# Kernel tuning notes

Hardware: AMD Instinct MI355X
Metric: run time of the kernel (lower is better)

The kernel has to match this reference:

```python
import jax, jax.numpy as jnp
import numpy as np

M, K, N = 32, 8192, 28672

def setup_inputs() -> dict:
    key = jax.random.key(0)
    k1, k2, k3 = jax.random.split(key, 3)
    act = jax.random.normal(k1, (M, K), dtype=jnp.float16)
    # int8 quantized weight, stored as int8 (spec lists int32 for harness compat)
    weight = jax.random.randint(k2, (K, N), -127, 128, dtype=jnp.int8)
    # per-output-channel dequant scale, small positive values typical of fp8/int8 quant
    scale = (jax.random.uniform(k3, (1, N), dtype=jnp.float32) * 0.01 + 1e-4).astype(jnp.float16)
    return {"act": act, "weight": weight, "scale": scale}

def reference(act, weight, scale):
    # grouped_gemm with single group: out[m,n] = (sum_k act[m,k] * w[k,n]) * scale[n]
    # int8 weight is dequantized inline; accumulate in fp32, emit fp16 like the kernel.
    acc = jnp.einsum("mk,kn->mn", act.astype(jnp.float16), weight.astype(jnp.float16),
                     preferred_element_type=jnp.float32)
    out = acc * scale.astype(jnp.float32)
    return out.astype(jnp.float16)
```

## Files before the change

### kernel.cpp

```cpp
#include <hip/hip_runtime.h>
#include <hip/hip_bf16.h>

#define MM 32
#define KK 8192
#define NN 28672
#define NB_COUNT (NN / 64)
#define REGION_BYTES (2048 * 64)

typedef _Float16 half8   __attribute__((ext_vector_type(8)));
typedef __fp16   fp16x2  __attribute__((ext_vector_type(2)));
typedef float    floatx4 __attribute__((ext_vector_type(4)));
typedef int      intx4   __attribute__((ext_vector_type(4)));
typedef unsigned int uintx2 __attribute__((ext_vector_type(2)));

__global__ __launch_bounds__(256) void act_cvt_kernel(
    const float* __restrict__ act, __fp16* __restrict__ act16)
{
    int i = (blockIdx.x * 256 + threadIdx.x) * 4;
    floatx4 v = *(const floatx4*)(act + i);
    fp16x2 lo = __builtin_amdgcn_cvt_pkrtz(v[0], v[1]);
    fp16x2 hi = __builtin_amdgcn_cvt_pkrtz(v[2], v[3]);
    __fp16* o = act16 + i;
    *(fp16x2*)(o)     = lo;
    *(fp16x2*)(o + 2) = hi;
}

__global__ __launch_bounds__(256) void repack_kernel(
    const int* __restrict__ weight, unsigned char* __restrict__ wpack)
{
    const int t    = threadIdx.x;
    const int slot = t & 63;
    const int kg   = t >> 6;
    const int n_base = blockIdx.x * 512 + slot * 8;
    const int k_base = blockIdx.y * 32 + kg * 8;

    const int* rp = weight + (size_t)k_base * NN + n_base;
    intx4 A[8], B[8];
#pragma unroll
    for (int j = 0; j < 8; ++j) {
        A[j] = *(const intx4*)(rp + (size_t)j * NN);
        B[j] = *(const intx4*)(rp + (size_t)j * NN + 4);
    }

    const int kc = k_base >> 11;
    const int s  = (k_base & 2047) >> 5;
    const int nb = n_base >> 6;
    const int wv = (n_base & 63) >> 4;
    const int c0 = n_base & 15;
    unsigned char* op = wpack
        + (((size_t)kc * NB_COUNT + nb) << 17)
        + (s << 11) + (wv << 9) + (kg << 7) + (c0 << 3);

    int d[16];
#pragma unroll
    for (int i = 0; i < 4; ++i) {
        d[2 * i]      = (A[0][i] & 255) | ((A[1][i] & 255) << 8) |
                        ((A[2][i] & 255) << 16) | (A[3][i] << 24);
        d[2 * i + 1]  = (A[4][i] & 255) | ((A[5][i] & 255) << 8) |
                        ((A[6][i] & 255) << 16) | (A[7][i] << 24);
        d[2 * i + 8]  = (B[0][i] & 255) | ((B[1][i] & 255) << 8) |
                        ((B[2][i] & 255) << 16) | (B[3][i] << 24);
        d[2 * i + 9]  = (B[4][i] & 255) | ((B[5][i] & 255) << 8) |
                        ((B[6][i] & 255) << 16) | (B[7][i] << 24);
    }
#pragma unroll
    for (int q = 0; q < 4; ++q) {
        intx4 v = {d[4 * q], d[4 * q + 1], d[4 * q + 2], d[4 * q + 3]};
        *(intx4*)(op + q * 16) = v;
    }
}

template <int KSPLIT>
__global__ __launch_bounds__(256) void gemm_pack_kernel(
    const __fp16*        __restrict__ act16,
    const unsigned char* __restrict__ wpack,
    float*               __restrict__ ws)
{
    const int lane = threadIdx.x & 63;
    const int wave = threadIdx.x >> 6;
    const int col  = lane & 15;
    const int quad = lane >> 4;

    const int nb  = blockIdx.x;
    const int kcb = blockIdx.y;
    const int kc  = kcb * (KK / KSPLIT);
    constexpr int NSTEP = (KK / KSPLIT) / 32;

    const unsigned char* wp = wpack
        + (((size_t)kcb * NB_COUNT + nb) << 17)
        + (wave << 9) + (lane << 3);
    const __fp16* ap0 = act16 + (size_t)col * KK + kc + quad * 8;
    const __fp16* ap1 = ap0 + (size_t)16 * KK;

    floatx4 acc0 = {0.f, 0.f, 0.f, 0.f};
    floatx4 acc1 = {0.f, 0.f, 0.f, 0.f};

    uintx2 wA, wB;
    half8  aA0, aA1, aB0, aB1;

    auto load_step = [&](int s, uintx2& w, half8& a0, half8& a1) {
        w  = *(const uintx2*)(wp + (size_t)s * 2048);
        a0 = *(const half8*)(ap0 + s * 32);
        a1 = *(const half8*)(ap1 + s * 32);
    };

    auto compute_step = [&](uintx2 w, const half8 a0, const half8 a1) {
        const unsigned lo = w[0], hi = w[1];
        int j0 = (int)(lo << 24) >> 24;
        int j1 = (int)(lo << 16) >> 24;
        int j2 = (int)(lo <<  8) >> 24;
        int j3 = (int)lo >> 24;
        int j4 = (int)(hi << 24) >> 24;
        int j5 = (int)(hi << 16) >> 24;
        int j6 = (int)(hi <<  8) >> 24;
        int j7 = (int)hi >> 24;
        fp16x2 p0 = __builtin_amdgcn_cvt_pkrtz((float)j0, (float)j1);
        fp16x2 p1 = __builtin_amdgcn_cvt_pkrtz((float)j2, (float)j3);
        fp16x2 p2 = __builtin_amdgcn_cvt_pkrtz((float)j4, (float)j5);
        fp16x2 p3 = __builtin_amdgcn_cvt_pkrtz((float)j6, (float)j7);
        half8 b;
        b[0] = p0[0]; b[1] = p0[1]; b[2] = p1[0]; b[3] = p1[1];
        b[4] = p2[0]; b[5] = p2[1]; b[6] = p3[0]; b[7] = p3[1];
        acc0 = __builtin_amdgcn_mfma_f32_16x16x32_f16(a0, b, acc0, 0, 0, 0);
        acc1 = __builtin_amdgcn_mfma_f32_16x16x32_f16(a1, b, acc1, 0, 0, 0);
    };

    load_step(0, wA, aA0, aA1);
#pragma unroll 1
    for (int s = 0; s < NSTEP / 2 - 1; ++s) {
        load_step(2 * s + 1, wB, aB0, aB1);
        compute_step(wA, aA0, aA1);
        load_step(2 * s + 2, wA, aA0, aA1);
        compute_step(wB, aB0, aB1);
    }
    load_step(NSTEP - 1, wB, aB0, aB1);
    compute_step(wA, aA0, aA1);
    compute_step(wB, aB0, aB1);

    float* wsb = ws + (size_t)kcb * MM * NN + nb * 64 + wave * 16 + col;
#pragma unroll
    for (int r = 0; r < 4; ++r) {
        int m0 = quad * 4 + r;
        wsb[(size_t)m0 * NN]        = acc0[r];
        wsb[(size_t)(m0 + 16) * NN] = acc1[r];
    }
}

template <int KSPLIT>
__global__ __launch_bounds__(256) void finalize_kernel(
    const float* __restrict__ ws,
    const float* __restrict__ scale,
    float*       __restrict__ out)
{
    const int n = blockIdx.x * 256 + threadIdx.x;
    const int m = blockIdx.y;
    float sum = 0.f;
#pragma unroll
    for (int c = 0; c < KSPLIT; ++c)
        sum += ws[(size_t)c * MM * NN + (size_t)m * NN + n];
    out[(size_t)m * NN + n] = sum * scale[n];
}

__global__ __launch_bounds__(256) void gemm_direct_kernel(
    const float* __restrict__ act,
    const int*   __restrict__ weight,
    const float* __restrict__ scale,
    float*       __restrict__ out)
{
    const int lane = threadIdx.x & 63;
    const int wave = threadIdx.x >> 6;
    const int col  = lane & 15;
    const int quad = lane >> 4;
    const int n0 = blockIdx.x * 64 + wave * 16 + col;

    floatx4 acc0 = {0.f, 0.f, 0.f, 0.f};
    floatx4 acc1 = {0.f, 0.f, 0.f, 0.f};
    const float* ap0 = act + (size_t)col * KK + quad * 8;
    const float* ap1 = ap0 + (size_t)16 * KK;
    const int* wp = weight + (size_t)(quad * 8) * NN + n0;

    for (int s = 0; s < KK / 32; ++s) {
        floatx4 a0lo = *(const floatx4*)(ap0);
        floatx4 a0hi = *(const floatx4*)(ap0 + 4);
        floatx4 a1lo = *(const floatx4*)(ap1);
        floatx4 a1hi = *(const floatx4*)(ap1 + 4);
        half8 a0, a1, b;
#pragma unroll
        for (int j = 0; j < 4; ++j) {
            a0[j] = (_Float16)a0lo[j]; a0[j + 4] = (_Float16)a0hi[j];
            a1[j] = (_Float16)a1lo[j]; a1[j + 4] = (_Float16)a1hi[j];
        }
#pragma unroll
        for (int j = 0; j < 8; ++j)
            b[j] = (_Float16)wp[(size_t)j * NN];
        acc0 = __builtin_amdgcn_mfma_f32_16x16x32_f16(a0, b, acc0, 0, 0, 0);
        acc1 = __builtin_amdgcn_mfma_f32_16x16x32_f16(a1, b, acc1, 0, 0, 0);
        ap0 += 32; ap1 += 32; wp += (size_t)32 * NN;
    }
    float sc = scale[n0];
#pragma unroll
    for (int r = 0; r < 4; ++r) {
        int m0 = quad * 4 + r;
        out[(size_t)m0 * NN + n0]        = acc0[r] * sc;
        out[(size_t)(m0 + 16) * NN + n0] = acc1[r] * sc;
    }
}

extern "C" void kernel_launch(void* const* d_in, const int* in_sizes, int n_in,
                              void* d_out, int out_size, void* d_ws, size_t ws_size,
                              hipStream_t stream)
{
    const float* act    = (const float*)d_in[0];
    const int*   weight = (const int*)d_in[1];
    const float* scale  = (const float*)d_in[2];
    float*       out    = (float*)d_out;

    constexpr int KSPLIT = 4;
    const size_t partials_bytes = (size_t)KSPLIT * MM * NN * sizeof(float);
    const size_t act16_off      = partials_bytes;
    const size_t wpack_off      = act16_off + (size_t)MM * KK * sizeof(__fp16);
    const size_t need           = wpack_off + (size_t)KK * NN;

    if (ws_size >= need) {
        float*         ws_part = (float*)d_ws;
        __fp16*        act16   = (__fp16*)((char*)d_ws + act16_off);
        unsigned char* wpack   = (unsigned char*)d_ws + wpack_off;

        act_cvt_kernel<<<MM * KK / (256 * 4), 256, 0, stream>>>(act, act16);

        dim3 rgrid(NN / 512, KK / 32);
        repack_kernel<<<rgrid, 256, 0, stream>>>(weight, wpack);

        dim3 ggrid(NB_COUNT, KSPLIT);
        gemm_pack_kernel<KSPLIT><<<ggrid, 256, 0, stream>>>(act16, wpack, ws_part);

        dim3 fgrid(NN / 256, MM);
        finalize_kernel<KSPLIT><<<fgrid, 256, 0, stream>>>(ws_part, scale, out);
    } else {
        gemm_direct_kernel<<<NN / 64, 256, 0, stream>>>(act, weight, scale, out);
    }
}
```

Measured before the change: 1.343 ms.

## Repack weights into 16-byte per-lane fragments covering two k-steps

Changes the packed int8 weight layout so each lane loads 16 bytes covering 64 k values, letting the GEMM issue one wider load per two MFMA k-steps. The repack kernel is restructured to a 512-block grid where each block sweeps all N columns for an 8-row k slice, reading rows with contiguous intx4 loads. This aims to cut load instruction count and improve memory efficiency in both the repack and the GEMM, at the cost of more registers per pipelined stage and fewer, longer-running repack blocks.

```diff
diff --git a/kernel.cpp b/kernel.cpp
--- a/kernel.cpp
+++ b/kernel.cpp
@@ -5,13 +5,11 @@
 #define KK 8192
 #define NN 28672
 #define NB_COUNT (NN / 64)
-#define REGION_BYTES (2048 * 64)
 
 typedef _Float16 half8   __attribute__((ext_vector_type(8)));
 typedef __fp16   fp16x2  __attribute__((ext_vector_type(2)));
 typedef float    floatx4 __attribute__((ext_vector_type(4)));
 typedef int      intx4   __attribute__((ext_vector_type(4)));
-typedef unsigned int uintx2 __attribute__((ext_vector_type(2)));
 
 __global__ __launch_bounds__(256) void act_cvt_kernel(
     const float* __restrict__ act, __fp16* __restrict__ act16)
@@ -25,48 +23,51 @@
     *(fp16x2*)(o + 2) = hi;
 }
 
+
 __global__ __launch_bounds__(256) void repack_kernel(
     const int* __restrict__ weight, unsigned char* __restrict__ wpack)
 {
-    const int t    = threadIdx.x;
-    const int slot = t & 63;
-    const int kg   = t >> 6;
-    const int n_base = blockIdx.x * 512 + slot * 8;
-    const int k_base = blockIdx.y * 32 + kg * 8;
-
-    const int* rp = weight + (size_t)k_base * NN + n_base;
-    intx4 A[8], B[8];
-#pragma unroll
-    for (int j = 0; j < 8; ++j) {
-        A[j] = *(const intx4*)(rp + (size_t)j * NN);
-        B[j] = *(const intx4*)(rp + (size_t)j * NN + 4);
-    }
-
-    const int kc = k_base >> 11;
-    const int s  = (k_base & 2047) >> 5;
-    const int nb = n_base >> 6;
-    const int wv = (n_base & 63) >> 4;
-    const int c0 = n_base & 15;
-    unsigned char* op = wpack
-        + (((size_t)kc * NB_COUNT + nb) << 17)
-        + (s << 11) + (wv << 9) + (kg << 7) + (c0 << 3);
-
-    int d[16];
-#pragma unroll
-    for (int i = 0; i < 4; ++i) {
-        d[2 * i]      = (A[0][i] & 255) | ((A[1][i] & 255) << 8) |
-                        ((A[2][i] & 255) << 16) | (A[3][i] << 24);
-        d[2 * i + 1]  = (A[4][i] & 255) | ((A[5][i] & 255) << 8) |
-                        ((A[6][i] & 255) << 16) | (A[7][i] << 24);
-        d[2 * i + 8]  = (B[0][i] & 255) | ((B[1][i] & 255) << 8) |
-                        ((B[2][i] & 255) << 16) | (B[3][i] << 24);
-        d[2 * i + 9]  = (B[4][i] & 255) | ((B[5][i] & 255) << 8) |
-                        ((B[6][i] & 255) << 16) | (B[7][i] << 24);
-    }
-#pragma unroll
-    for (int q = 0; q < 4; ++q) {
-        intx4 v = {d[4 * q], d[4 * q + 1], d[4 * q + 2], d[4 * q + 3]};
-        *(intx4*)(op + q * 16) = v;
+    const int t   = threadIdx.x;
+    const int ss  = blockIdx.x >> 2;
+    const int q   = blockIdx.x & 3;
+    const int kcb = ss >> 5;
+    const int ssl = ss & 31;
+    const int k0  = ss * 64 + q * 8;
+
+    const int* r0 = weight + (size_t)k0 * NN;
+    const int* r1 = r0 + (size_t)32 * NN;
+
+    for (int i = 0; i < 28; ++i) {
+        const int idx  = i * 256 + t;
+        const int nofs = idx * 4;
+
+        intx4 a[8], b[8];
+#pragma unroll
+        for (int j = 0; j < 8; ++j) {
+            a[j] = *(const intx4*)(r0 + (size_t)j * NN + nofs);
+            b[j] = *(const intx4*)(r1 + (size_t)j * NN + nofs);
+        }
+
+        const int nb   = nofs >> 6;
+        const int wn   = (nofs >> 4) & 3;
+        const int col0 = nofs & 15;
+        unsigned char* up = wpack
+            + (((size_t)kcb * NB_COUNT + nb) << 17)
+            + (ssl << 12) + (q << 10) + (wn << 8) + (col0 << 4);
+
+#pragma unroll
+        for (int ii = 0; ii < 4; ++ii) {
+            int d0 = (a[0][ii] & 255) | ((a[1][ii] & 255) << 8) |
+                     ((a[2][ii] & 255) << 16) | (a[3][ii] << 24);
+            int d1 = (a[4][ii] & 255) | ((a[5][ii] & 255) << 8) |
+                     ((a[6][ii] & 255) << 16) | (a[7][ii] << 24);
+            int d2 = (b[0][ii] & 255) | ((b[1][ii] & 255) << 8) |
+                     ((b[2][ii] & 255) << 16) | (b[3][ii] << 24);
+            int d3 = (b[4][ii] & 255) | ((b[5][ii] & 255) << 8) |
+                     ((b[6][ii] & 255) << 16) | (b[7][ii] << 24);
+            intx4 u = {d0, d1, d2, d3};
+            *(intx4*)(up + 16 * ii) = u;
+        }
     }
 }
 
@@ -84,28 +85,30 @@
     const int nb  = blockIdx.x;
     const int kcb = blockIdx.y;
     const int kc  = kcb * (KK / KSPLIT);
-    constexpr int NSTEP = (KK / KSPLIT) / 32;
+    constexpr int NSS = (KK / KSPLIT) / 64;
 
     const unsigned char* wp = wpack
         + (((size_t)kcb * NB_COUNT + nb) << 17)
-        + (wave << 9) + (lane << 3);
+        + (quad << 10) + (wave << 8) + (col << 4);
     const __fp16* ap0 = act16 + (size_t)col * KK + kc + quad * 8;
     const __fp16* ap1 = ap0 + (size_t)16 * KK;
 
     floatx4 acc0 = {0.f, 0.f, 0.f, 0.f};
     floatx4 acc1 = {0.f, 0.f, 0.f, 0.f};
 
-    uintx2 wA, wB;
-    half8  aA0, aA1, aB0, aB1;
-
-    auto load_step = [&](int s, uintx2& w, half8& a0, half8& a1) {
-        w  = *(const uintx2*)(wp + (size_t)s * 2048);
-        a0 = *(const half8*)(ap0 + s * 32);
-        a1 = *(const half8*)(ap1 + s * 32);
+    intx4 wA, wB;
+    half8 aA00, aA01, aA10, aA11, aB00, aB01, aB10, aB11;
+
+    auto load_step = [&](int s, intx4& wq, half8& a00, half8& a01,
+                         half8& a10, half8& a11) {
+        wq  = *(const intx4*)(wp + ((size_t)s << 12));
+        a00 = *(const half8*)(ap0 + s * 64);
+        a01 = *(const half8*)(ap0 + s * 64 + 32);
+        a10 = *(const half8*)(ap1 + s * 64);
+        a11 = *(const half8*)(ap1 + s * 64 + 32);
     };
 
-    auto compute_step = [&](uintx2 w, const half8 a0, const half8 a1) {
-        const unsigned lo = w[0], hi = w[1];
+    auto bfrag = [](unsigned lo, unsigned hi) -> half8 {
         int j0 = (int)(lo << 24) >> 24;
         int j1 = (int)(lo << 16) >> 24;
         int j2 = (int)(lo <<  8) >> 24;
@@ -121,21 +124,30 @@
         half8 b;
         b[0] = p0[0]; b[1] = p0[1]; b[2] = p1[0]; b[3] = p1[1];
         b[4] = p2[0]; b[5] = p2[1]; b[6] = p3[0]; b[7] = p3[1];
-        acc0 = __builtin_amdgcn_mfma_f32_16x16x32_f16(a0, b, acc0, 0, 0, 0);
-        acc1 = __builtin_amdgcn_mfma_f32_16x16x32_f16(a1, b, acc1, 0, 0, 0);
+        return b;
     };
 
-    load_step(0, wA, aA0, aA1);
+    auto compute_step = [&](const intx4 wq, const half8 a00, const half8 a01,
+                            const half8 a10, const half8 a11) {
+        half8 bh0 = bfrag((unsigned)wq[0], (unsigned)wq[1]);
+        half8 bh1 = bfrag((unsigned)wq[2], (unsigned)wq[3]);
+        acc0 = __builtin_amdgcn_mfma_f32_16x16x32_f16(a00, bh0, acc0, 0, 0, 0);
+        acc1 = __builtin_amdgcn_mfma_f32_16x16x32_f16(a10, bh0, acc1, 0, 0, 0);
+        acc0 = __builtin_amdgcn_mfma_f32_16x16x32_f16(a01, bh1, acc0, 0, 0, 0);
+        acc1 = __builtin_amdgcn_mfma_f32_16x16x32_f16(a11, bh1, acc1, 0, 0, 0);
+    };
+
+    load_step(0, wA, aA00, aA01, aA10, aA11);
 #pragma unroll 1
-    for (int s = 0; s < NSTEP / 2 - 1; ++s) {
-        load_step(2 * s + 1, wB, aB0, aB1);
-        compute_step(wA, aA0, aA1);
-        load_step(2 * s + 2, wA, aA0, aA1);
-        compute_step(wB, aB0, aB1);
-    }
-    load_step(NSTEP - 1, wB, aB0, aB1);
-    compute_step(wA, aA0, aA1);
-    compute_step(wB, aB0, aB1);
+    for (int s = 0; s < NSS / 2 - 1; ++s) {
+        load_step(2 * s + 1, wB, aB00, aB01, aB10, aB11);
+        compute_step(wA, aA00, aA01, aA10, aA11);
+        load_step(2 * s + 2, wA, aA00, aA01, aA10, aA11);
+        compute_step(wB, aB00, aB01, aB10, aB11);
+    }
+    load_step(NSS - 1, wB, aB00, aB01, aB10, aB11);
+    compute_step(wA, aA00, aA01, aA10, aA11);
+    compute_step(wB, aB00, aB01, aB10, aB11);
 
     float* wsb = ws + (size_t)kcb * MM * NN + nb * 64 + wave * 16 + col;
 #pragma unroll
@@ -228,8 +240,7 @@
 
         act_cvt_kernel<<<MM * KK / (256 * 4), 256, 0, stream>>>(act, act16);
 
-        dim3 rgrid(NN / 512, KK / 32);
-        repack_kernel<<<rgrid, 256, 0, stream>>>(weight, wpack);
+        repack_kernel<<<512, 256, 0, stream>>>(weight, wpack);
 
         dim3 ggrid(NB_COUNT, KSPLIT);
         gemm_pack_kernel<KSPLIT><<<ggrid, 256, 0, stream>>>(act16, wpack, ws_part);
```

After: 1.328 ms. No clear change (-1.1%).
